# Kernel tuning notes

Hardware: AMD Instinct MI355X
Metric: run time of the kernel (lower is better)

## Reference

```python
import jax, jax.numpy as jnp
import numpy as np

B, P, F = 16, 100000, 200000

def setup_inputs() -> dict:
    key = jax.random.key(0)
    k1, k2, k3, k4, k5, k6 = jax.random.split(key, 6)
    points = jax.random.normal(k1, (B, P, 3), dtype=jnp.float32)
    tfcolor = jax.random.uniform(k2, (B, P, 3), dtype=jnp.float32)
    faces = jax.random.randint(k3, (1, F, 3), 0, P, dtype=jnp.int64)
    cam_rot = jax.random.normal(k4, (B, 3, 3), dtype=jnp.float32)
    cam_pos = jax.random.normal(k5, (B, 3), dtype=jnp.float32)
    cam_proj = jax.random.uniform(k6, (1, 3, 1), dtype=jnp.float32)
    return {"points_bxpx3": points, "tfcolor_bxpx3": tfcolor, "faces_fx3": faces,
            "cameras_1": cam_rot, "cameras_2": cam_pos, "cameras_3": cam_proj}

def reference(points_bxpx3, tfcolor_bxpx3, faces_fx3, cameras_1, cameras_2, cameras_3):
    faces = faces_fx3[0]                               # [F,3]
    rot_t = jnp.swapaxes(cameras_1, 1, 2)              # [B,3,3] transpose
    pts = points_bxpx3 - cameras_2[:, None, :]         # camera-space translate
    pts = jnp.matmul(pts, rot_t)                       # [B,P,3] rotate
    proj = cameras_3[0].reshape(1, 1, 3)               # [1,1,3]
    xy3 = pts * proj
    xy = xy3[..., :2] / xy3[..., 2:3]                  # perspective divide [B,P,2]
    # per-face vertex gathers
    pf0 = pts[:, faces[:, 0], :]
    pf1 = pts[:, faces[:, 1], :]
    pf2 = pts[:, faces[:, 2], :]
    points3d_bxfx9 = jnp.concatenate((pf0, pf1, pf2), axis=2)
    points2d_bxfx6 = jnp.concatenate((xy[:, faces[:, 0], :], xy[:, faces[:, 1], :], xy[:, faces[:, 2], :]), axis=2)
    normal = jnp.cross(pf1 - pf0, pf2 - pf0)           # [B,F,3]
    normalz_bxfx1 = normal[..., 2:3]
    normallen = jnp.sqrt(jnp.sum(normal * normal, axis=2, keepdims=True))
    normal1_bxfx3 = normal / (normallen + 1e-15)
    tfcolor_bxfx9 = jnp.concatenate((tfcolor_bxpx3[:, faces[:, 0], :], tfcolor_bxpx3[:, faces[:, 1], :], tfcolor_bxpx3[:, faces[:, 2], :]), axis=2)
    # func is an external rasterizer callback; modeled as identity passthrough
    return (points3d_bxfx9, points2d_bxfx6, normalz_bxfx1, tfcolor_bxfx9, normal1_bxfx3)
```

## Files before the change

### kernel.cpp

```cpp
#include <hip/hip_runtime.h>


constexpr int Bn = 16;
constexpr int Pn = 100000;
constexpr int Fn = 200000;
constexpr int ChunksPerB = (Fn + 255) / 256;

constexpr size_t O0 = 0;
constexpr size_t O1 = (size_t)Bn * Fn * 9;
constexpr size_t O2 = O1 + (size_t)Bn * Fn * 6;
constexpr size_t O3 = O2 + (size_t)Bn * Fn * 1;
constexpr size_t O4 = O3 + (size_t)Bn * Fn * 9;

typedef float floatx4 __attribute__((ext_vector_type(4)));

struct V3 { float x, y, z; };

__device__ __forceinline__ float dot3_blas(float a0, float a1, float a2,
                                           float b0, float b1, float b2) {
    return fmaf(a2, b2, fmaf(a1, b1, __fmul_rn(a0, b0)));
}

__device__ __forceinline__ void flush4(float* __restrict__ dst,
                                       const float* __restrict__ src,
                                       int nfloats, int tid) {
    const floatx4* s4 = (const floatx4*)src;
    floatx4* d4 = (floatx4*)dst;
    const int n4 = nfloats >> 2;
    for (int i = tid; i < n4; i += 256)
        __builtin_nontemporal_store(s4[i], &d4[i]);
}

__global__ __launch_bounds__(256, 8)
void render_mesh_kernel(const float* __restrict__ points,
                        const float* __restrict__ tfcolor,
                        const int*   __restrict__ faces,
                        const float* __restrict__ cam_rot,
                        const float* __restrict__ cam_pos,
                        const float* __restrict__ cam_proj,
                        float* __restrict__ out)
{
    __shared__ __align__(16) float s3d[256 * 9];
    __shared__ __align__(16) float s2d[256 * 6];
    __shared__ __align__(16) float snz[256];
    __shared__ __align__(16) float sn1[256 * 3];

    const int blid = blockIdx.x;
    const int xcd  = blid & 7;
    const int s    = blid >> 3;
    const int b    = xcd + 8 * (s / ChunksPerB);
    const int blockStart = (s % ChunksPerB) * 256;

    const int t = threadIdx.x;
    const int f = blockStart + t;
    const int nvalid = min(256, Fn - blockStart);

    float col[3][3];

    if (f < Fn) {
        const int i0 = faces[f * 3 + 0];
        const int i1 = faces[f * 3 + 1];
        const int i2 = faces[f * 3 + 2];

        const V3* pb = (const V3*)(points  + (size_t)b * Pn * 3);
        const V3* cb = (const V3*)(tfcolor + (size_t)b * Pn * 3);

        const V3 p0 = pb[i0], p1 = pb[i1], p2 = pb[i2];
        const V3 c0v = cb[i0], c1v = cb[i1], c2v = cb[i2];

        const float r00 = cam_rot[b * 9 + 0], r01 = cam_rot[b * 9 + 1], r02 = cam_rot[b * 9 + 2];
        const float r10 = cam_rot[b * 9 + 3], r11 = cam_rot[b * 9 + 4], r12 = cam_rot[b * 9 + 5];
        const float r20 = cam_rot[b * 9 + 6], r21 = cam_rot[b * 9 + 7], r22 = cam_rot[b * 9 + 8];
        const float cp0 = cam_pos[b * 3 + 0], cp1 = cam_pos[b * 3 + 1], cp2 = cam_pos[b * 3 + 2];
        const float pj0 = cam_proj[0], pj1 = cam_proj[1], pj2 = cam_proj[2];

        const V3 pv[3] = {p0, p1, p2};
        col[0][0] = c0v.x; col[0][1] = c0v.y; col[0][2] = c0v.z;
        col[1][0] = c1v.x; col[1][1] = c1v.y; col[1][2] = c1v.z;
        col[2][0] = c2v.x; col[2][1] = c2v.y; col[2][2] = c2v.z;

        float px[3][3];
#pragma unroll
        for (int v = 0; v < 3; ++v) {
            const float dx = __fsub_rn(pv[v].x, cp0);
            const float dy = __fsub_rn(pv[v].y, cp1);
            const float dz = __fsub_rn(pv[v].z, cp2);
            const float tx = dot3_blas(dx, dy, dz, r00, r01, r02);
            const float ty = dot3_blas(dx, dy, dz, r10, r11, r12);
            const float tz = dot3_blas(dx, dy, dz, r20, r21, r22);
            px[v][0] = tx; px[v][1] = ty; px[v][2] = tz;
            s3d[t * 9 + v * 3 + 0] = tx;
            s3d[t * 9 + v * 3 + 1] = ty;
            s3d[t * 9 + v * 3 + 2] = tz;
            const float zv = __fmul_rn(tz, pj2);
            s2d[t * 6 + v * 2 + 0] = __fdiv_rn(__fmul_rn(tx, pj0), zv);
            s2d[t * 6 + v * 2 + 1] = __fdiv_rn(__fmul_rn(ty, pj1), zv);
        }

        const float e1x = px[1][0] - px[0][0], e1y = px[1][1] - px[0][1], e1z = px[1][2] - px[0][2];
        const float e2x = px[2][0] - px[0][0], e2y = px[2][1] - px[0][1], e2z = px[2][2] - px[0][2];
        const float nx = e1y * e2z - e1z * e2y;
        const float ny = e1z * e2x - e1x * e2z;
        const float nz = e1x * e2y - e1y * e2x;
        const float len = sqrtf(nx * nx + ny * ny + nz * nz);
        const float inv = 1.0f / (len + 1e-15f);

        snz[t] = nz;
        sn1[t * 3 + 0] = nx * inv;
        sn1[t * 3 + 1] = ny * inv;
        sn1[t * 3 + 2] = nz * inv;
    }

    __syncthreads();

    const size_t bf0 = (size_t)b * Fn + blockStart;
    flush4(out + O0 + bf0 * 9, s3d, nvalid * 9, t);
    flush4(out + O1 + bf0 * 6, s2d, nvalid * 6, t);
    flush4(out + O2 + bf0 * 1, snz, nvalid * 1, t);
    flush4(out + O4 + bf0 * 3, sn1, nvalid * 3, t);

    __syncthreads();

    if (f < Fn) {
#pragma unroll
        for (int v = 0; v < 3; ++v) {
            s3d[t * 9 + v * 3 + 0] = col[v][0];
            s3d[t * 9 + v * 3 + 1] = col[v][1];
            s3d[t * 9 + v * 3 + 2] = col[v][2];
        }
    }
    __syncthreads();
    flush4(out + O3 + bf0 * 9, s3d, nvalid * 9, t);
}

extern "C" void kernel_launch(void* const* d_in, const int* in_sizes, int n_in,
                              void* d_out, int out_size, void* d_ws, size_t ws_size,
                              hipStream_t stream) {
    const float* points   = (const float*)d_in[0];
    const float* tfcolor  = (const float*)d_in[1];
    const int*   faces    = (const int*)d_in[2];
    const float* cam_rot  = (const float*)d_in[3];
    const float* cam_pos  = (const float*)d_in[4];
    const float* cam_proj = (const float*)d_in[5];
    float* out = (float*)d_out;

    dim3 block(256);
    dim3 grid(Bn * ChunksPerB);
    render_mesh_kernel<<<grid, block, 0, stream>>>(points, tfcolor, faces,
                                                   cam_rot, cam_pos, cam_proj, out);
}
```

Measured before the change: 103.1 us.

## Split fused mesh kernel into separate points and colors kernels

Splits the single kernel into two launches: one gathers points and computes the projection, 2D coordinates and normals, and the other gathers colors and writes them out. The aim is to cut per-block shared memory and register pressure and to shorten each block's critical path, which could raise occupancy. In exchange, the faces indices are read twice, there is a second launch, and the two gather phases no longer overlap inside one block.

```diff
diff --git a/kernel.cpp b/kernel.cpp
--- a/kernel.cpp
+++ b/kernel.cpp
@@ -31,42 +31,40 @@
         __builtin_nontemporal_store(s4[i], &d4[i]);
 }
 
+__device__ __forceinline__ void decode_block(int blid, int& b, int& blockStart) {
+    const int xcd = blid & 7;
+    const int s   = blid >> 3;
+    b = xcd + 8 * (s / ChunksPerB);
+    blockStart = (s % ChunksPerB) * 256;
+}
+
 __global__ __launch_bounds__(256, 8)
-void render_mesh_kernel(const float* __restrict__ points,
-                        const float* __restrict__ tfcolor,
-                        const int*   __restrict__ faces,
-                        const float* __restrict__ cam_rot,
-                        const float* __restrict__ cam_pos,
-                        const float* __restrict__ cam_proj,
-                        float* __restrict__ out)
+void points_kernel(const float* __restrict__ points,
+                   const int*   __restrict__ faces,
+                   const float* __restrict__ cam_rot,
+                   const float* __restrict__ cam_pos,
+                   const float* __restrict__ cam_proj,
+                   float* __restrict__ out)
 {
     __shared__ __align__(16) float s3d[256 * 9];
     __shared__ __align__(16) float s2d[256 * 6];
     __shared__ __align__(16) float snz[256];
     __shared__ __align__(16) float sn1[256 * 3];
 
-    const int blid = blockIdx.x;
-    const int xcd  = blid & 7;
-    const int s    = blid >> 3;
-    const int b    = xcd + 8 * (s / ChunksPerB);
-    const int blockStart = (s % ChunksPerB) * 256;
+    int b, blockStart;
+    decode_block(blockIdx.x, b, blockStart);
 
     const int t = threadIdx.x;
     const int f = blockStart + t;
     const int nvalid = min(256, Fn - blockStart);
-
-    float col[3][3];
 
     if (f < Fn) {
         const int i0 = faces[f * 3 + 0];
         const int i1 = faces[f * 3 + 1];
         const int i2 = faces[f * 3 + 2];
 
-        const V3* pb = (const V3*)(points  + (size_t)b * Pn * 3);
-        const V3* cb = (const V3*)(tfcolor + (size_t)b * Pn * 3);
-
+        const V3* pb = (const V3*)(points + (size_t)b * Pn * 3);
         const V3 p0 = pb[i0], p1 = pb[i1], p2 = pb[i2];
-        const V3 c0v = cb[i0], c1v = cb[i1], c2v = cb[i2];
 
         const float r00 = cam_rot[b * 9 + 0], r01 = cam_rot[b * 9 + 1], r02 = cam_rot[b * 9 + 2];
         const float r10 = cam_rot[b * 9 + 3], r11 = cam_rot[b * 9 + 4], r12 = cam_rot[b * 9 + 5];
@@ -75,10 +73,6 @@
         const float pj0 = cam_proj[0], pj1 = cam_proj[1], pj2 = cam_proj[2];
 
         const V3 pv[3] = {p0, p1, p2};
-        col[0][0] = c0v.x; col[0][1] = c0v.y; col[0][2] = c0v.z;
-        col[1][0] = c1v.x; col[1][1] = c1v.y; col[1][2] = c1v.z;
-        col[2][0] = c2v.x; col[2][1] = c2v.y; col[2][2] = c2v.z;
-
         float px[3][3];
 #pragma unroll
         for (int v = 0; v < 3; ++v) {
@@ -118,19 +112,39 @@
     flush4(out + O1 + bf0 * 6, s2d, nvalid * 6, t);
     flush4(out + O2 + bf0 * 1, snz, nvalid * 1, t);
     flush4(out + O4 + bf0 * 3, sn1, nvalid * 3, t);
+}
+
+__global__ __launch_bounds__(256, 8)
+void colors_kernel(const float* __restrict__ tfcolor,
+                   const int*   __restrict__ faces,
+                   float* __restrict__ out)
+{
+    __shared__ __align__(16) float scl[256 * 9];
+
+    int b, blockStart;
+    decode_block(blockIdx.x, b, blockStart);
+
+    const int t = threadIdx.x;
+    const int f = blockStart + t;
+    const int nvalid = min(256, Fn - blockStart);
+
+    if (f < Fn) {
+        const int i0 = faces[f * 3 + 0];
+        const int i1 = faces[f * 3 + 1];
+        const int i2 = faces[f * 3 + 2];
+
+        const V3* cb = (const V3*)(tfcolor + (size_t)b * Pn * 3);
+        const V3 c0v = cb[i0], c1v = cb[i1], c2v = cb[i2];
+
+        scl[t * 9 + 0] = c0v.x; scl[t * 9 + 1] = c0v.y; scl[t * 9 + 2] = c0v.z;
+        scl[t * 9 + 3] = c1v.x; scl[t * 9 + 4] = c1v.y; scl[t * 9 + 5] = c1v.z;
+        scl[t * 9 + 6] = c2v.x; scl[t * 9 + 7] = c2v.y; scl[t * 9 + 8] = c2v.z;
+    }
 
     __syncthreads();
 
-    if (f < Fn) {
-#pragma unroll
-        for (int v = 0; v < 3; ++v) {
-            s3d[t * 9 + v * 3 + 0] = col[v][0];
-            s3d[t * 9 + v * 3 + 1] = col[v][1];
-            s3d[t * 9 + v * 3 + 2] = col[v][2];
-        }
-    }
-    __syncthreads();
-    flush4(out + O3 + bf0 * 9, s3d, nvalid * 9, t);
+    const size_t bf0 = (size_t)b * Fn + blockStart;
+    flush4(out + O3 + bf0 * 9, scl, nvalid * 9, t);
 }
 
 extern "C" void kernel_launch(void* const* d_in, const int* in_sizes, int n_in,
@@ -146,6 +160,7 @@
 
     dim3 block(256);
     dim3 grid(Bn * ChunksPerB);
-    render_mesh_kernel<<<grid, block, 0, stream>>>(points, tfcolor, faces,
-                                                   cam_rot, cam_pos, cam_proj, out);
+    points_kernel<<<grid, block, 0, stream>>>(points, faces, cam_rot,
+                                              cam_pos, cam_proj, out);
+    colors_kernel<<<grid, block, 0, stream>>>(tfcolor, faces, out);
 }
```

Result: slower. 106.6 us (+3.4%).

## Precompute per-vertex transforms into interleaved workspace, then gather per face

Applied to the files above, without the earlier changes.

Adds a pre-pass kernel that transforms every vertex once per batch and writes a 32-byte record (camera-space xyz, projected xy, color) into a workspace laid out vertex-major with all 16 batches adjacent. The face kernel then assigns 16 faces × 16 batches per block, so one vertex index gathers contiguous records across batches. This avoids recomputing each vertex transform per face and gives coalesced gathers. In exchange it needs a second launch, writes and rereads about 51 MB of workspace, and uses strided output flushes across batches. The old kernel stays as a fallback when the workspace is too small.

```diff
diff --git a/kernel.cpp b/kernel.cpp
--- a/kernel.cpp
+++ b/kernel.cpp
@@ -12,6 +12,8 @@
 constexpr size_t O3 = O2 + (size_t)Bn * Fn * 1;
 constexpr size_t O4 = O3 + (size_t)Bn * Fn * 9;
 
+constexpr size_t REC_BYTES = (size_t)Pn * Bn * 8 * sizeof(float);
+
 typedef float floatx4 __attribute__((ext_vector_type(4)));
 
 struct V3 { float x, y, z; };
@@ -21,9 +23,128 @@
     return fmaf(a2, b2, fmaf(a1, b1, __fmul_rn(a0, b0)));
 }
 
-__device__ __forceinline__ void flush4(float* __restrict__ dst,
-                                       const float* __restrict__ src,
-                                       int nfloats, int tid) {
+__global__ __launch_bounds__(256)
+void transformT_kernel(const float* __restrict__ points,
+                       const float* __restrict__ tfcolor,
+                       const float* __restrict__ cam_rot,
+                       const float* __restrict__ cam_pos,
+                       const float* __restrict__ cam_proj,
+                       floatx4* __restrict__ rec)
+{
+    const int t  = threadIdx.x;
+    const int b  = t & 15;
+    const int lp = t >> 4;
+    const int p  = blockIdx.x * 16 + lp;
+    if (p >= Pn) return;
+
+    const float r00 = cam_rot[b * 9 + 0], r01 = cam_rot[b * 9 + 1], r02 = cam_rot[b * 9 + 2];
+    const float r10 = cam_rot[b * 9 + 3], r11 = cam_rot[b * 9 + 4], r12 = cam_rot[b * 9 + 5];
+    const float r20 = cam_rot[b * 9 + 6], r21 = cam_rot[b * 9 + 7], r22 = cam_rot[b * 9 + 8];
+    const float cp0 = cam_pos[b * 3 + 0], cp1 = cam_pos[b * 3 + 1], cp2 = cam_pos[b * 3 + 2];
+    const float pj0 = cam_proj[0], pj1 = cam_proj[1], pj2 = cam_proj[2];
+
+    const V3 pt = ((const V3*)(points  + (size_t)b * Pn * 3))[p];
+    const V3 cl = ((const V3*)(tfcolor + (size_t)b * Pn * 3))[p];
+
+    const float dx = __fsub_rn(pt.x, cp0);
+    const float dy = __fsub_rn(pt.y, cp1);
+    const float dz = __fsub_rn(pt.z, cp2);
+    const float tx = dot3_blas(dx, dy, dz, r00, r01, r02);
+    const float ty = dot3_blas(dx, dy, dz, r10, r11, r12);
+    const float tz = dot3_blas(dx, dy, dz, r20, r21, r22);
+    const float zv = __fmul_rn(tz, pj2);
+    const float x0 = __fdiv_rn(__fmul_rn(tx, pj0), zv);
+    const float x1 = __fdiv_rn(__fmul_rn(ty, pj1), zv);
+
+    floatx4 ra = {tx, ty, tz, x0};
+    floatx4 rb = {x1, cl.x, cl.y, cl.z};
+    floatx4* r4 = rec + ((size_t)p * 16 + b) * 2;
+    r4[0] = ra;
+    r4[1] = rb;
+}
+
+constexpr int S9 = 148;
+constexpr int S6 = 100;
+constexpr int S1 = 20;
+constexpr int S3 = 52;
+
+template<int N4PerB, int SrcStride, int DstStride4>
+__device__ __forceinline__ void flushT(floatx4* __restrict__ d4,
+                                       const float* __restrict__ s, int tid) {
+    constexpr int total = N4PerB * 16;
+    for (int j = tid; j < total; j += 256) {
+        const int b = j / N4PerB;
+        const int k = j - b * N4PerB;
+        __builtin_nontemporal_store(*(const floatx4*)(s + b * SrcStride + k * 4),
+                                    &d4[(size_t)b * DstStride4 + k]);
+    }
+}
+
+__global__ __launch_bounds__(256)
+void faceT_kernel(const int* __restrict__ faces,
+                  const floatx4* __restrict__ rec,
+                  float* __restrict__ out)
+{
+    __shared__ __align__(16) float s3d[16 * S9];
+    __shared__ __align__(16) float s2d[16 * S6];
+    __shared__ __align__(16) float snz[16 * S1];
+    __shared__ __align__(16) float scl[16 * S9];
+    __shared__ __align__(16) float sn1[16 * S3];
+
+    const int t  = threadIdx.x;
+    const int b  = t & 15;
+    const int fl = t >> 4;
+    const int f0 = blockIdx.x * 16;
+    const int f  = f0 + fl;
+
+    const int i0 = faces[f * 3 + 0];
+    const int i1 = faces[f * 3 + 1];
+    const int i2 = faces[f * 3 + 2];
+    const int idxs[3] = {i0, i1, i2};
+
+    float px[3][3];
+#pragma unroll
+    for (int v = 0; v < 3; ++v) {
+        const size_t base = ((size_t)idxs[v] * 16 + b) * 2;
+        const floatx4 va = rec[base + 0];
+        const floatx4 vb = rec[base + 1];
+        px[v][0] = va.x; px[v][1] = va.y; px[v][2] = va.z;
+        s3d[b * S9 + fl * 9 + v * 3 + 0] = va.x;
+        s3d[b * S9 + fl * 9 + v * 3 + 1] = va.y;
+        s3d[b * S9 + fl * 9 + v * 3 + 2] = va.z;
+        s2d[b * S6 + fl * 6 + v * 2 + 0] = va.w;
+        s2d[b * S6 + fl * 6 + v * 2 + 1] = vb.x;
+        scl[b * S9 + fl * 9 + v * 3 + 0] = vb.y;
+        scl[b * S9 + fl * 9 + v * 3 + 1] = vb.z;
+        scl[b * S9 + fl * 9 + v * 3 + 2] = vb.w;
+    }
+
+    const float e1x = px[1][0] - px[0][0], e1y = px[1][1] - px[0][1], e1z = px[1][2] - px[0][2];
+    const float e2x = px[2][0] - px[0][0], e2y = px[2][1] - px[0][1], e2z = px[2][2] - px[0][2];
+    const float nx = e1y * e2z - e1z * e2y;
+    const float ny = e1z * e2x - e1x * e2z;
+    const float nz = e1x * e2y - e1y * e2x;
+    const float len = sqrtf(nx * nx + ny * ny + nz * nz);
+    const float inv = 1.0f / (len + 1e-15f);
+
+    snz[b * S1 + fl] = nz;
+    sn1[b * S3 + fl * 3 + 0] = nx * inv;
+    sn1[b * S3 + fl * 3 + 1] = ny * inv;
+    sn1[b * S3 + fl * 3 + 2] = nz * inv;
+
+    __syncthreads();
+
+    const int bid = blockIdx.x;
+    flushT<36, S9, 450000>((floatx4*)(out + O0) + (size_t)bid * 36, s3d, t);
+    flushT<24, S6, 300000>((floatx4*)(out + O1) + (size_t)bid * 24, s2d, t);
+    flushT< 4, S1,  50000>((floatx4*)(out + O2) + (size_t)bid *  4, snz, t);
+    flushT<36, S9, 450000>((floatx4*)(out + O3) + (size_t)bid * 36, scl, t);
+    flushT<12, S3, 150000>((floatx4*)(out + O4) + (size_t)bid * 12, sn1, t);
+}
+
+__device__ __forceinline__ void flush4f(float* __restrict__ dst,
+                                        const float* __restrict__ src,
+                                        int nfloats, int tid) {
     const floatx4* s4 = (const floatx4*)src;
     floatx4* d4 = (floatx4*)dst;
     const int n4 = nfloats >> 2;
@@ -32,13 +153,13 @@
 }
 
 __global__ __launch_bounds__(256, 8)
-void render_mesh_kernel(const float* __restrict__ points,
-                        const float* __restrict__ tfcolor,
-                        const int*   __restrict__ faces,
-                        const float* __restrict__ cam_rot,
-                        const float* __restrict__ cam_pos,
-                        const float* __restrict__ cam_proj,
-                        float* __restrict__ out)
+void render_mesh_fallback(const float* __restrict__ points,
+                          const float* __restrict__ tfcolor,
+                          const int*   __restrict__ faces,
+                          const float* __restrict__ cam_rot,
+                          const float* __restrict__ cam_pos,
+                          const float* __restrict__ cam_proj,
+                          float* __restrict__ out)
 {
     __shared__ __align__(16) float s3d[256 * 9];
     __shared__ __align__(16) float s2d[256 * 6];
@@ -64,7 +185,6 @@
 
         const V3* pb = (const V3*)(points  + (size_t)b * Pn * 3);
         const V3* cb = (const V3*)(tfcolor + (size_t)b * Pn * 3);
-
         const V3 p0 = pb[i0], p1 = pb[i1], p2 = pb[i2];
         const V3 c0v = cb[i0], c1v = cb[i1], c2v = cb[i2];
 
@@ -114,10 +234,10 @@
     __syncthreads();
 
     const size_t bf0 = (size_t)b * Fn + blockStart;
-    flush4(out + O0 + bf0 * 9, s3d, nvalid * 9, t);
-    flush4(out + O1 + bf0 * 6, s2d, nvalid * 6, t);
-    flush4(out + O2 + bf0 * 1, snz, nvalid * 1, t);
-    flush4(out + O4 + bf0 * 3, sn1, nvalid * 3, t);
+    flush4f(out + O0 + bf0 * 9, s3d, nvalid * 9, t);
+    flush4f(out + O1 + bf0 * 6, s2d, nvalid * 6, t);
+    flush4f(out + O2 + bf0 * 1, snz, nvalid * 1, t);
+    flush4f(out + O4 + bf0 * 3, sn1, nvalid * 3, t);
 
     __syncthreads();
 
@@ -130,7 +250,7 @@
         }
     }
     __syncthreads();
-    flush4(out + O3 + bf0 * 9, s3d, nvalid * 9, t);
+    flush4f(out + O3 + bf0 * 9, s3d, nvalid * 9, t);
 }
 
 extern "C" void kernel_launch(void* const* d_in, const int* in_sizes, int n_in,
@@ -144,8 +264,14 @@
     const float* cam_proj = (const float*)d_in[5];
     float* out = (float*)d_out;
 
-    dim3 block(256);
-    dim3 grid(Bn * ChunksPerB);
-    render_mesh_kernel<<<grid, block, 0, stream>>>(points, tfcolor, faces,
-                                                   cam_rot, cam_pos, cam_proj, out);
-}
+    if (ws_size >= REC_BYTES) {
+        floatx4* rec = (floatx4*)d_ws;
+        transformT_kernel<<<dim3(Pn / 16), 256, 0, stream>>>(points, tfcolor,
+                                                             cam_rot, cam_pos,
+                                                             cam_proj, rec);
+        faceT_kernel<<<dim3(Fn / 16), 256, 0, stream>>>(faces, rec, out);
+    } else {
+        render_mesh_fallback<<<dim3(Bn * ChunksPerB), 256, 0, stream>>>(
+            points, tfcolor, faces, cam_rot, cam_pos, cam_proj, out);
+    }
+}
```

Measured after the change: 120.6 us. 16.9% more time.
